# Performance work log

Hardware: AMD Instinct MI355X
Metric: run time of the kernel (lower is better)

Reference implementation:

```python
import jax, jax.numpy as jnp
import numpy as np

# Static pyramid config (must match setup_inputs' source_shape / level_start)
LEVEL_SHAPES = [(100, 100), (50, 50), (25, 25), (13, 13)]
DIM = 256
N_HEAD = 8
HEAD_DIM = DIM // N_HEAD
N_LEVEL = 4
N_POINT = 4
DIM_FF = 1024
B = 8
Q = 2048
LEN_IN = sum(h * w for h, w in LEVEL_SHAPES)


def layer_norm(x, g, b, eps=1e-5):
    m = jnp.mean(x, axis=-1, keepdims=True)
    v = jnp.mean(jnp.square(x - m), axis=-1, keepdims=True)
    return (x - m) * jax.lax.rsqrt(v + eps) * g + b


def bilinear_sample(v_flat, loc, H, W):
    # v_flat: (BH, H*W, hd); loc: (BH, Q, P, 2) normalized [0,1] as (x, y)
    # grid_sample align_corners=False with zero padding: pixel = loc*size - 0.5
    x = loc[..., 0] * W - 0.5
    y = loc[..., 1] * H - 0.5
    x0 = jnp.floor(x)
    y0 = jnp.floor(y)
    wx = (x - x0)[..., None]
    wy = (y - y0)[..., None]
    x0i = x0.astype(jnp.int32)
    y0i = y0.astype(jnp.int32)

    def gather(xi, yi):
        valid = ((xi >= 0) & (xi < W) & (yi >= 0) & (yi < H)).astype(v_flat.dtype)
        idx = jnp.clip(yi, 0, H - 1) * W + jnp.clip(xi, 0, W - 1)  # (BH,Q,P)
        BH, Qq, P = idx.shape
        f = jnp.take_along_axis(v_flat, idx.reshape(BH, Qq * P, 1), axis=1)
        return f.reshape(BH, Qq, P, -1) * valid[..., None]

    g00 = gather(x0i, y0i)
    g01 = gather(x0i + 1, y0i)
    g10 = gather(x0i, y0i + 1)
    g11 = gather(x0i + 1, y0i + 1)
    top = g00 * (1.0 - wx) + g01 * wx
    bot = g10 * (1.0 - wx) + g11 * wx
    return top * (1.0 - wy) + bot * wy


def ms_deform_attn_core(value, loc, attn):
    # value: (B, Lin, nh, hd); loc: (B, Q, nh, L, P, 2); attn: (B, Q, nh, L, P)
    Bv, Lin, nh, hd = value.shape
    Qq = loc.shape[1]
    out = jnp.zeros((Bv * nh, Qq, hd), value.dtype)
    start = 0
    for l, (H, W) in enumerate(LEVEL_SHAPES):
        v = value[:, start:start + H * W]                       # (B, HW, nh, hd)
        v = v.transpose(0, 2, 1, 3).reshape(Bv * nh, H * W, hd)
        ll = loc[:, :, :, l].transpose(0, 2, 1, 3, 4).reshape(Bv * nh, Qq, N_POINT, 2)
        aa = attn[:, :, :, l].transpose(0, 2, 1, 3).reshape(Bv * nh, Qq, N_POINT, 1)
        samp = bilinear_sample(v, ll, H, W)                     # (B*nh, Q, P, hd)
        out = out + jnp.sum(samp * aa, axis=2)
        start += H * W
    return out.reshape(Bv, nh, Qq, hd).transpose(0, 2, 1, 3).reshape(Bv, Qq, nh * hd)


def setup_inputs() -> dict:
    key = jax.random.key(0)
    ks = jax.random.split(key, 24)
    std = 0.02
    inp = {
        'input': jax.random.normal(ks[0], (B, Q, DIM), jnp.float32),
        'pos': jax.random.normal(ks[1], (B, Q, DIM), jnp.float32),
        'reference_point': jax.random.uniform(ks[2], (B, Q, N_LEVEL, 2), jnp.float32),
        'source': jax.random.normal(ks[3], (B, LEN_IN, DIM), jnp.float32),
        'source_shape': jnp.array(LEVEL_SHAPES, jnp.int64),
        'level_start': jnp.array(np.cumsum([0] + [h * w for h, w in LEVEL_SHAPES[:-1]]), jnp.int64),
        'source_mask': jnp.zeros((B, LEN_IN), jnp.bool_),
        # LayerNorms
        'ln1_g': jnp.ones((DIM,), jnp.float32), 'ln1_b': jnp.zeros((DIM,), jnp.float32),
        'ln2_g': jnp.ones((DIM,), jnp.float32), 'ln2_b': jnp.zeros((DIM,), jnp.float32),
        # MSDeformAttn projections
        'Wv': std * jax.random.normal(ks[4], (DIM, DIM), jnp.float32), 'bv': jnp.zeros((DIM,), jnp.float32),
        'Woff': std * jax.random.normal(ks[5], (DIM, N_HEAD * N_LEVEL * N_POINT * 2), jnp.float32),
        'boff': 0.5 * jax.random.normal(ks[6], (N_HEAD * N_LEVEL * N_POINT * 2,), jnp.float32),
        'Wattn': std * jax.random.normal(ks[7], (DIM, N_HEAD * N_LEVEL * N_POINT), jnp.float32),
        'battn': jnp.zeros((N_HEAD * N_LEVEL * N_POINT,), jnp.float32),
        'Wout': std * jax.random.normal(ks[8], (DIM, DIM), jnp.float32), 'bout': jnp.zeros((DIM,), jnp.float32),
        # FFN
        'W1': std * jax.random.normal(ks[9], (DIM, DIM_FF), jnp.float32), 'b1': jnp.zeros((DIM_FF,), jnp.float32),
        'W2': std * jax.random.normal(ks[10], (DIM_FF, DIM), jnp.float32), 'b2': jnp.zeros((DIM,), jnp.float32),
    }
    return inp


def reference(input, pos, reference_point, source, source_shape, level_start, source_mask,
              ln1_g, ln1_b, ln2_g, ln2_b, Wv, bv, Woff, boff, Wattn, battn, Wout, bout,
              W1, b1, W2, b2):
    # ---- cross norm + pos ----
    q = layer_norm(input, ln1_g, ln1_b)
    qp = q + pos
    # ---- MSDeformAttn ----
    value = source @ Wv + bv
    value = jnp.where(source_mask[..., None], 0.0, value)
    value = value.reshape(B, LEN_IN, N_HEAD, HEAD_DIM)
    offsets = (qp @ Woff + boff).reshape(B, Q, N_HEAD, N_LEVEL, N_POINT, 2)
    attn = (qp @ Wattn + battn).reshape(B, Q, N_HEAD, N_LEVEL * N_POINT)
    attn = jax.nn.softmax(attn, axis=-1).reshape(B, Q, N_HEAD, N_LEVEL, N_POINT)
    # offset normalizer is (W, H) per level
    normalizer = jnp.array([[w, h] for h, w in LEVEL_SHAPES], jnp.float32)
    loc = reference_point[:, :, None, :, None, :] + offsets / normalizer[None, None, None, :, None, :]
    out = ms_deform_attn_core(value, loc, attn)
    out = out @ Wout + bout
    x = input + out  # dropout is identity in eval
    # ---- FFN ----
    h = layer_norm(x, ln2_g, ln2_b)
    h = jax.nn.relu(h @ W1 + b1) @ W2 + b2
    x = x + h
    return (x, loc)
```

## Files before the change

kernel.cpp:

```cpp
#include <hip/hip_runtime.h>
#include <hip/hip_bf16.h>
#include <cstdint>
#include <cstddef>

#define B_    8
#define Q_    2048
#define DIM_  256
#define NH    8
#define HD    32
#define NL    4
#define NP    4
#define DFF   1024
#define LEN_IN_ 13294
#define MV    (B_*LEN_IN_)
#define MVPAD 106368
#define MQ    (B_*Q_)

typedef unsigned short u16;
typedef unsigned int   u32;
typedef __attribute__((ext_vector_type(8))) short short8;
typedef __attribute__((ext_vector_type(4))) float f32x4v;
typedef __attribute__((ext_vector_type(4))) unsigned short u16x4;

static __device__ __forceinline__ u16 f2bf(float f){
  union { float f; unsigned u; } x; x.f = f;
  unsigned r = x.u + 0x7fffu + ((x.u >> 16) & 1u);
  return (u16)(r >> 16);
}

#define GLDS(gp, lp) __builtin_amdgcn_global_load_lds( \
    (const __attribute__((address_space(1))) void*)(gp), \
    (__attribute__((address_space(3))) void*)(lp), 16, 0, 0)

template<int EPI, bool AF32>
__global__ __launch_bounds__(512, 4)
void gemm_k(const void* __restrict__ Ap, const u16* __restrict__ Bt,
            const float* __restrict__ bias, const float* __restrict__ res,
            void* __restrict__ outp, int N, int K, int Mstore)
{
  __shared__ u16 As[2][128*64];
  __shared__ u16 Bs[2][128*64];
  const int t = threadIdx.x;
  const int l = t & 63, wid = t >> 6;
  const int wm = wid >> 2, wn = wid & 3;
  const int m0 = blockIdx.x * 128, n0 = blockIdx.y * 128;

  f32x4v acc[4][2];
#pragma unroll
  for (int i = 0; i < 4; ++i)
#pragma unroll
    for (int j = 0; j < 2; ++j) acc[i][j] = 0.f;

  const int nkt = K >> 6;

  {
    float4 pa[4];
#pragma unroll
    for (int i = 0; i < 2; ++i) {
      const int chunk = i * 512 + t;
      const int row = chunk >> 3;
      const int sc = (chunk & 7) ^ (row & 7);
      if (AF32) {
        const int gr = m0 + row;
        float4 z = {0.f, 0.f, 0.f, 0.f};
        pa[2*i] = z; pa[2*i+1] = z;
        if (gr < Mstore) {
          const float* ga = (const float*)Ap + (size_t)gr * K + sc * 8;
          pa[2*i]   = *reinterpret_cast<const float4*>(ga);
          pa[2*i+1] = *reinterpret_cast<const float4*>(ga + 4);
        }
      } else {
        const u16* ga = (const u16*)Ap + (size_t)(m0 + row) * K + sc * 8;
        GLDS(ga, As[0] + chunk * 8);
      }
      const u16* gb = Bt + (size_t)(n0 + row) * K + sc * 8;
      GLDS(gb, Bs[0] + chunk * 8);
    }
    if (AF32) {
#pragma unroll
      for (int i = 0; i < 2; ++i) {
        const int chunk = i * 512 + t;
        short8 pk;
        pk[0]=(short)f2bf(pa[2*i].x);   pk[1]=(short)f2bf(pa[2*i].y);
        pk[2]=(short)f2bf(pa[2*i].z);   pk[3]=(short)f2bf(pa[2*i].w);
        pk[4]=(short)f2bf(pa[2*i+1].x); pk[5]=(short)f2bf(pa[2*i+1].y);
        pk[6]=(short)f2bf(pa[2*i+1].z); pk[7]=(short)f2bf(pa[2*i+1].w);
        *reinterpret_cast<short8*>(As[0] + chunk * 8) = pk;
      }
    }
    __syncthreads();
  }

  int cur = 0;
  for (int kt = 0; kt < nkt; ++kt) {
    const bool pf = (kt + 1 < nkt);
    float4 pa[4];
    if (pf) {
      const int kn = (kt + 1) * 64;
#pragma unroll
      for (int i = 0; i < 2; ++i) {
        const int chunk = i * 512 + t;
        const int row = chunk >> 3;
        const int sc = (chunk & 7) ^ (row & 7);
        if (AF32) {
          const int gr = m0 + row;
          float4 z = {0.f, 0.f, 0.f, 0.f};
          pa[2*i] = z; pa[2*i+1] = z;
          if (gr < Mstore) {
            const float* ga = (const float*)Ap + (size_t)gr * K + kn + sc * 8;
            pa[2*i]   = *reinterpret_cast<const float4*>(ga);
            pa[2*i+1] = *reinterpret_cast<const float4*>(ga + 4);
          }
        } else {
          const u16* ga = (const u16*)Ap + (size_t)(m0 + row) * K + kn + sc * 8;
          GLDS(ga, As[cur ^ 1] + chunk * 8);
        }
        const u16* gb = Bt + (size_t)(n0 + row) * K + kn + sc * 8;
        GLDS(gb, Bs[cur ^ 1] + chunk * 8);
      }
    }
#pragma unroll
    for (int kk = 0; kk < 2; ++kk) {
      short8 af[4], bfr[2];
      const int lr  = l & 15;
      const int c   = kk * 4 + (l >> 4);
      const int swz = c ^ (lr & 7);
#pragma unroll
      for (int mi = 0; mi < 4; ++mi) {
        int r = wm * 64 + mi * 16 + lr;
        af[mi] = *reinterpret_cast<const short8*>(As[cur] + (r * 8 + swz) * 8);
      }
#pragma unroll
      for (int ni = 0; ni < 2; ++ni) {
        int r = wn * 32 + ni * 16 + lr;
        bfr[ni] = *reinterpret_cast<const short8*>(Bs[cur] + (r * 8 + swz) * 8);
      }
#pragma unroll
      for (int mi = 0; mi < 4; ++mi)
#pragma unroll
        for (int ni = 0; ni < 2; ++ni)
          acc[mi][ni] = __builtin_amdgcn_mfma_f32_16x16x32_bf16(af[mi], bfr[ni], acc[mi][ni], 0, 0, 0);
    }
    if (pf && AF32) {
#pragma unroll
      for (int i = 0; i < 2; ++i) {
        const int chunk = i * 512 + t;
        short8 pk;
        pk[0]=(short)f2bf(pa[2*i].x);   pk[1]=(short)f2bf(pa[2*i].y);
        pk[2]=(short)f2bf(pa[2*i].z);   pk[3]=(short)f2bf(pa[2*i].w);
        pk[4]=(short)f2bf(pa[2*i+1].x); pk[5]=(short)f2bf(pa[2*i+1].y);
        pk[6]=(short)f2bf(pa[2*i+1].z); pk[7]=(short)f2bf(pa[2*i+1].w);
        *reinterpret_cast<short8*>(As[cur ^ 1] + chunk * 8) = pk;
      }
    }
    __syncthreads();
    cur ^= 1;
  }

  const int lr4 = l >> 4;
#pragma unroll
  for (int mi = 0; mi < 4; ++mi) {
    int rowb = m0 + wm * 64 + mi * 16 + lr4 * 4;
#pragma unroll
    for (int ni = 0; ni < 2; ++ni) {
      int col = n0 + wn * 32 + ni * 16 + (l & 15);
      float bb = bias[col];
#pragma unroll
      for (int v = 0; v < 4; ++v) {
        int r = rowb + v;
        if (r < Mstore) {
          float cv = acc[mi][ni][v] + bb;
          if (EPI == 2) cv += res[(size_t)r * N + col];
          if (EPI == 3) cv = fmaxf(cv, 0.f);
          if (EPI == 0 || EPI == 2) ((float*)outp)[(size_t)r * N + col] = cv;
          else                      ((u16*)outp)[(size_t)r * N + col] = f2bf(cv);
        }
      }
    }
  }
}

__global__ void prep_weights(const float* __restrict__ Wv,   const float* __restrict__ Woff,
                             const float* __restrict__ Wattn,const float* __restrict__ Wout,
                             const float* __restrict__ W1,   const float* __restrict__ W2,
                             const float* __restrict__ boff, const float* __restrict__ battn,
                             u16* __restrict__ WvT, u16* __restrict__ WcombT,
                             u16* __restrict__ WoutT, u16* __restrict__ W1T,
                             u16* __restrict__ W2T, float* __restrict__ bcomb)
{
  const int gid = blockIdx.x * 256 + threadIdx.x;
  const int R0 = 65536, R1 = R0 + 98304, R2 = R1 + 65536, R3 = R2 + 262144,
            R4 = R3 + 262144, R5 = R4 + 384;
  if (gid < R0) {
    int n = gid >> 8, k = gid & 255;
    WvT[gid] = f2bf(Wv[(size_t)k * 256 + n]);
  } else if (gid < R1) {
    int lo = gid - R0, n = lo >> 8, k = lo & 255;
    float s = (n < 256) ? Woff[(size_t)k * 256 + n] : Wattn[(size_t)k * 128 + (n - 256)];
    WcombT[lo] = f2bf(s);
  } else if (gid < R2) {
    int lo = gid - R1, n = lo >> 8, k = lo & 255;
    WoutT[lo] = f2bf(Wout[(size_t)k * 256 + n]);
  } else if (gid < R3) {
    int lo = gid - R2, n = lo >> 8, k = lo & 255;
    W1T[lo] = f2bf(W1[(size_t)k * 1024 + n]);
  } else if (gid < R4) {
    int lo = gid - R3, n = lo >> 10, k = lo & 1023;
    W2T[lo] = f2bf(W2[(size_t)k * 256 + n]);
  } else if (gid < R5) {
    int lo = gid - R4;
    bcomb[lo] = (lo < 256) ? boff[lo] : battn[lo - 256];
  }
}

template<bool ADDPOS>
__global__ __launch_bounds__(256)
void ln_k(const float* __restrict__ x, const float* __restrict__ pos,
          const float* __restrict__ g, const float* __restrict__ b, u16* __restrict__ out)
{
  const int warp = threadIdx.x >> 6, l = threadIdx.x & 63;
  const int row = blockIdx.x * 4 + warp;
  const float4 xv = reinterpret_cast<const float4*>(x + (size_t)row * 256)[l];
  float s = xv.x + xv.y + xv.z + xv.w;
#pragma unroll
  for (int o = 32; o; o >>= 1) s += __shfl_xor(s, o);
  const float mean = s * (1.f / 256.f);
  const float d0 = xv.x - mean, d1 = xv.y - mean, d2 = xv.z - mean, d3 = xv.w - mean;
  float vs = d0 * d0 + d1 * d1 + d2 * d2 + d3 * d3;
#pragma unroll
  for (int o = 32; o; o >>= 1) vs += __shfl_xor(vs, o);
  const float rs = rsqrtf(vs * (1.f / 256.f) + 1e-5f);
  const float4 gv = reinterpret_cast<const float4*>(g)[l];
  const float4 bv = reinterpret_cast<const float4*>(b)[l];
  float o0 = d0 * rs * gv.x + bv.x;
  float o1 = d1 * rs * gv.y + bv.y;
  float o2 = d2 * rs * gv.z + bv.z;
  float o3 = d3 * rs * gv.w + bv.w;
  if (ADDPOS) {
    const float4 pv = reinterpret_cast<const float4*>(pos + (size_t)row * 256)[l];
    o0 += pv.x; o1 += pv.y; o2 += pv.z; o3 += pv.w;
  }
  u16x4 ov; ov.x = f2bf(o0); ov.y = f2bf(o1); ov.z = f2bf(o2); ov.w = f2bf(o3);
  reinterpret_cast<u16x4*>(out + (size_t)row * 256)[l] = ov;
}

__global__ __launch_bounds__(256)
void msdeform_k(const u16* __restrict__ value, const float* __restrict__ oa,
                const float* __restrict__ refpt, float* __restrict__ locout,
                u16* __restrict__ outp)
{
  const int t = threadIdx.x;
  const int rloc = t >> 7;
  const int rem = t & 127;
  const int h = rem >> 4, p = rem & 15;
  const int row = blockIdx.x * 2 + rloc;
  const int b = row >> 11;
  const int lv = p >> 2;
  const float* orow = oa + (size_t)row * 384;

  const float araw = orow[256 + h * 16 + p];
  float mx = araw;
#pragma unroll
  for (int o = 1; o < 16; o <<= 1) mx = fmaxf(mx, __shfl_xor(mx, o, 16));
  const float e = __expf(araw - mx);
  float se = e;
#pragma unroll
  for (int o = 1; o < 16; o <<= 1) se += __shfl_xor(se, o, 16);
  const float aw = e / se;

  const float2 off = *reinterpret_cast<const float2*>(orow + h * 32 + p * 2);
  const float rn = (lv == 0) ? (1.f / 100.f) : (lv == 1) ? (1.f / 50.f)
                 : (lv == 2) ? (1.f / 25.f) : (1.f / 13.f);
  const float rx = refpt[(size_t)row * 8 + lv * 2 + 0];
  const float ry = refpt[(size_t)row * 8 + lv * 2 + 1];
  const float lx = rx + off.x * rn;
  const float ly = ry + off.y * rn;
  float2 lw; lw.x = lx; lw.y = ly;
  *reinterpret_cast<float2*>(locout + (((size_t)row * 8 + h) * 16 + p) * 2) = lw;

  const int Wl = (lv == 0) ? 100 : (lv == 1) ? 50 : (lv == 2) ? 25 : 13;
  const int st = (lv == 0) ? 0 : (lv == 1) ? 10000 : (lv == 2) ? 12500 : 13125;
  const float Wf = (float)Wl;
  const float xx = lx * Wf - 0.5f, yy = ly * Wf - 0.5f;
  const float xf = floorf(xx), yf = floorf(yy);
  const float wx = xx - xf, wy = yy - yf;
  const int x0 = (int)xf, y0 = (int)yf;
  const int xc0 = min(max(x0, 0), Wl - 1), xc1 = min(max(x0 + 1, 0), Wl - 1);
  const int yc0 = min(max(y0, 0), Wl - 1), yc1 = min(max(y0 + 1, 0), Wl - 1);
  const float vx0 = (x0 >= 0 && x0 < Wl) ? 1.f : 0.f;
  const float vx1 = (x0 + 1 >= 0 && x0 + 1 < Wl) ? 1.f : 0.f;
  const float vy0 = (y0 >= 0 && y0 < Wl) ? 1.f : 0.f;
  const float vy1 = (y0 + 1 >= 0 && y0 + 1 < Wl) ? 1.f : 0.f;
  const int o00 = st + yc0 * Wl + xc0, o01 = st + yc0 * Wl + xc1;
  const int o10 = st + yc1 * Wl + xc0, o11 = st + yc1 * Wl + xc1;
  const float w00 = aw * (1.f - wx) * (1.f - wy) * vx0 * vy0;
  const float w01 = aw * wx * (1.f - wy) * vx1 * vy0;
  const float w10 = aw * (1.f - wx) * wy * vx0 * vy1;
  const float w11 = aw * wx * wy * vx1 * vy1;

  const char* vbase = (const char*)value + (size_t)b * LEN_IN_ * 512 + (size_t)(h * 32 + p * 2) * 2;
  float a0 = 0.f, a1 = 0.f;
#pragma unroll
  for (int q = 0; q < 16; ++q) {
    const int   c00 = __shfl(o00, q, 16), c01 = __shfl(o01, q, 16);
    const int   c10 = __shfl(o10, q, 16), c11 = __shfl(o11, q, 16);
    const float u00 = __shfl(w00, q, 16), u01 = __shfl(w01, q, 16);
    const float u10 = __shfl(w10, q, 16), u11 = __shfl(w11, q, 16);
    const u32 g00 = *reinterpret_cast<const u32*>(vbase + (size_t)c00 * 512);
    const u32 g01 = *reinterpret_cast<const u32*>(vbase + (size_t)c01 * 512);
    const u32 g10 = *reinterpret_cast<const u32*>(vbase + (size_t)c10 * 512);
    const u32 g11 = *reinterpret_cast<const u32*>(vbase + (size_t)c11 * 512);
    union { u32 u; float f; } lo, hi;
    lo.u = g00 << 16; hi.u = g00 & 0xffff0000u; a0 += u00 * lo.f; a1 += u00 * hi.f;
    lo.u = g01 << 16; hi.u = g01 & 0xffff0000u; a0 += u01 * lo.f; a1 += u01 * hi.f;
    lo.u = g10 << 16; hi.u = g10 & 0xffff0000u; a0 += u10 * lo.f; a1 += u10 * hi.f;
    lo.u = g11 << 16; hi.u = g11 & 0xffff0000u; a0 += u11 * lo.f; a1 += u11 * hi.f;
  }
  const u32 res = ((u32)f2bf(a1) << 16) | (u32)f2bf(a0);
  reinterpret_cast<u32*>(outp)[(size_t)row * 128 + h * 16 + p] = res;
}

extern "C" void kernel_launch(void* const* d_in, const int* in_sizes, int n_in,
                              void* d_out, int out_size, void* d_ws, size_t ws_size,
                              hipStream_t stream)
{
  (void)in_sizes; (void)n_in; (void)out_size; (void)ws_size;
  const float* input  = (const float*)d_in[0];
  const float* pos    = (const float*)d_in[1];
  const float* refpt  = (const float*)d_in[2];
  const float* source = (const float*)d_in[3];
  const float* ln1_g  = (const float*)d_in[7];
  const float* ln1_b  = (const float*)d_in[8];
  const float* ln2_g  = (const float*)d_in[9];
  const float* ln2_b  = (const float*)d_in[10];
  const float* Wv     = (const float*)d_in[11];
  const float* bv     = (const float*)d_in[12];
  const float* Woff   = (const float*)d_in[13];
  const float* boff   = (const float*)d_in[14];
  const float* Wattn  = (const float*)d_in[15];
  const float* battn  = (const float*)d_in[16];
  const float* Wout   = (const float*)d_in[17];
  const float* bout   = (const float*)d_in[18];
  const float* W1     = (const float*)d_in[19];
  const float* b1     = (const float*)d_in[20];
  const float* W2     = (const float*)d_in[21];
  const float* b2     = (const float*)d_in[22];

  char* ws = (char*)d_ws;
  u16*   WvT    = (u16*)  (ws + 0);
  u16*   WcombT = (u16*)  (ws + 131072);
  u16*   WoutT  = (u16*)  (ws + 327680);
  u16*   W1T    = (u16*)  (ws + 458752);
  u16*   W2T    = (u16*)  (ws + 983040);
  float* bcomb  = (float*)(ws + 1507328);
  u16*   valueB = (u16*)  (ws + 1508864);
  u16*   hB     = (u16*)  (ws + 1508864);
  u16*   qpB    = (u16*)  (ws + 55969280);
  u16*   msout  = (u16*)  (ws + 55969280);
  float* oa     = (float*)(ws + 64357888);
  float* xbuf   = (float*)(ws + 89523712);
  u16*   xnB    = (u16*)  (ws + 106300928);

  float* out_x   = (float*)d_out;
  float* out_loc = (float*)d_out + (size_t)MQ * DIM_;

  hipLaunchKernelGGL(prep_weights, dim3(2946), dim3(256), 0, stream,
                     Wv, Woff, Wattn, Wout, W1, W2, boff, battn,
                     WvT, WcombT, WoutT, W1T, W2T, bcomb);

  hipLaunchKernelGGL((ln_k<true>), dim3(MQ / 4), dim3(256), 0, stream, input, pos, ln1_g, ln1_b, qpB);

  hipLaunchKernelGGL((gemm_k<1, true>), dim3(MVPAD / 128, 2), dim3(512), 0, stream,
                     (const void*)source, WvT, bv, (const float*)nullptr, (void*)valueB, 256, 256, MV);

  hipLaunchKernelGGL((gemm_k<0, false>), dim3(MQ / 128, 3), dim3(512), 0, stream,
                     (const void*)qpB, WcombT, bcomb, (const float*)nullptr, (void*)oa, 384, 256, MQ);

  hipLaunchKernelGGL(msdeform_k, dim3(MQ / 2), dim3(256), 0, stream,
                     valueB, oa, refpt, out_loc, msout);

  hipLaunchKernelGGL((gemm_k<2, false>), dim3(MQ / 128, 2), dim3(512), 0, stream,
                     (const void*)msout, WoutT, bout, input, (void*)xbuf, 256, 256, MQ);

  hipLaunchKernelGGL((ln_k<false>), dim3(MQ / 4), dim3(256), 0, stream, xbuf, (const float*)nullptr, ln2_g, ln2_b, xnB);

  hipLaunchKernelGGL((gemm_k<3, false>), dim3(MQ / 128, DFF / 128), dim3(512), 0, stream,
                     (const void*)xnB, W1T, b1, (const float*)nullptr, (void*)hB, DFF, 256, MQ);

  hipLaunchKernelGGL((gemm_k<2, false>), dim3(MQ / 128, 2), dim3(512), 0, stream,
                     (const void*)hB, W2T, b2, xbuf, (void*)out_x, 256, 1024, MQ);
}
```

Before: 413.7 us.

## Load A fragments directly to registers and stage B in large K chunks

The GEMM no longer stages A through LDS. Each lane loads its MFMA A fragment straight from global memory into registers and prefetches the next 32-wide K slice. B is staged into a single 128x256 LDS buffer per 256-wide K chunk, which cuts the number of barriers. This removes LDS traffic and sync for A, but the A global loads are now strided, B loads are no longer double-buffered, and the kernel waits on vmcnt(0) before each chunk.

```diff
diff --git a/kernel.cpp b/kernel.cpp
--- a/kernel.cpp
+++ b/kernel.cpp
@@ -38,11 +38,11 @@
             const float* __restrict__ bias, const float* __restrict__ res,
             void* __restrict__ outp, int N, int K, int Mstore)
 {
-  __shared__ u16 As[2][128*64];
-  __shared__ u16 Bs[2][128*64];
+  __shared__ u16 Bs[128 * 256];
   const int t = threadIdx.x;
   const int l = t & 63, wid = t >> 6;
   const int wm = wid >> 2, wn = wid & 3;
+  const int lr = l & 15, hi = l >> 4;
   const int m0 = blockIdx.x * 128, n0 = blockIdx.y * 128;
 
   f32x4v acc[4][2];
@@ -51,89 +51,85 @@
 #pragma unroll
     for (int j = 0; j < 2; ++j) acc[i][j] = 0.f;
 
-  const int nkt = K >> 6;
-
-  {
-    float4 pa[4];
-#pragma unroll
-    for (int i = 0; i < 2; ++i) {
+  const u16*   pA16[4];
+  const float* pA32[4];
+#pragma unroll
+  for (int mi = 0; mi < 4; ++mi) {
+    int r = m0 + wm * 64 + mi * 16 + lr;
+    r = (r < Mstore) ? r : (Mstore - 1);
+    if (AF32) pA32[mi] = (const float*)Ap + (size_t)r * K + hi * 8;
+    else      pA16[mi] = (const u16*)Ap + (size_t)r * K + hi * 8;
+  }
+
+  const int nchunk = K >> 8;
+  const int S = K >> 5;
+
+  short8 af[4];
+  short8 afn[4];
+  float4 pan[8];
+
+  if (AF32) {
+#pragma unroll
+    for (int mi = 0; mi < 4; ++mi) {
+      pan[2*mi]   = *reinterpret_cast<const float4*>(pA32[mi]);
+      pan[2*mi+1] = *reinterpret_cast<const float4*>(pA32[mi] + 4);
+    }
+  } else {
+#pragma unroll
+    for (int mi = 0; mi < 4; ++mi)
+      afn[mi] = *reinterpret_cast<const short8*>(pA16[mi]);
+  }
+
+  for (int ck = 0; ck < nchunk; ++ck) {
+    if (ck) __syncthreads();
+#pragma unroll
+    for (int i = 0; i < 8; ++i) {
       const int chunk = i * 512 + t;
-      const int row = chunk >> 3;
-      const int sc = (chunk & 7) ^ (row & 7);
+      const int row = chunk >> 5;
+      const int c16 = chunk & 31;
+      const int sc  = c16 ^ (row & 7);
+      GLDS(Bt + (size_t)(n0 + row) * K + ck * 256 + sc * 8, Bs + chunk * 8);
+    }
+    asm volatile("s_waitcnt vmcnt(0)" ::: "memory");
+    __syncthreads();
+
+#pragma unroll
+    for (int sl = 0; sl < 8; ++sl) {
+      const int s = ck * 8 + sl;
       if (AF32) {
-        const int gr = m0 + row;
-        float4 z = {0.f, 0.f, 0.f, 0.f};
-        pa[2*i] = z; pa[2*i+1] = z;
-        if (gr < Mstore) {
-          const float* ga = (const float*)Ap + (size_t)gr * K + sc * 8;
-          pa[2*i]   = *reinterpret_cast<const float4*>(ga);
-          pa[2*i+1] = *reinterpret_cast<const float4*>(ga + 4);
+#pragma unroll
+        for (int mi = 0; mi < 4; ++mi) {
+          short8 pk;
+          pk[0]=(short)f2bf(pan[2*mi].x);   pk[1]=(short)f2bf(pan[2*mi].y);
+          pk[2]=(short)f2bf(pan[2*mi].z);   pk[3]=(short)f2bf(pan[2*mi].w);
+          pk[4]=(short)f2bf(pan[2*mi+1].x); pk[5]=(short)f2bf(pan[2*mi+1].y);
+          pk[6]=(short)f2bf(pan[2*mi+1].z); pk[7]=(short)f2bf(pan[2*mi+1].w);
+          af[mi] = pk;
         }
       } else {
-        const u16* ga = (const u16*)Ap + (size_t)(m0 + row) * K + sc * 8;
-        GLDS(ga, As[0] + chunk * 8);
+#pragma unroll
+        for (int mi = 0; mi < 4; ++mi) af[mi] = afn[mi];
       }
-      const u16* gb = Bt + (size_t)(n0 + row) * K + sc * 8;
-      GLDS(gb, Bs[0] + chunk * 8);
-    }
-    if (AF32) {
-#pragma unroll
-      for (int i = 0; i < 2; ++i) {
-        const int chunk = i * 512 + t;
-        short8 pk;
-        pk[0]=(short)f2bf(pa[2*i].x);   pk[1]=(short)f2bf(pa[2*i].y);
-        pk[2]=(short)f2bf(pa[2*i].z);   pk[3]=(short)f2bf(pa[2*i].w);
-        pk[4]=(short)f2bf(pa[2*i+1].x); pk[5]=(short)f2bf(pa[2*i+1].y);
-        pk[6]=(short)f2bf(pa[2*i+1].z); pk[7]=(short)f2bf(pa[2*i+1].w);
-        *reinterpret_cast<short8*>(As[0] + chunk * 8) = pk;
-      }
-    }
-    __syncthreads();
-  }
-
-  int cur = 0;
-  for (int kt = 0; kt < nkt; ++kt) {
-    const bool pf = (kt + 1 < nkt);
-    float4 pa[4];
-    if (pf) {
-      const int kn = (kt + 1) * 64;
-#pragma unroll
-      for (int i = 0; i < 2; ++i) {
-        const int chunk = i * 512 + t;
-        const int row = chunk >> 3;
-        const int sc = (chunk & 7) ^ (row & 7);
+      if (s + 1 < S) {
+        const int ko = (s + 1) * 32;
         if (AF32) {
-          const int gr = m0 + row;
-          float4 z = {0.f, 0.f, 0.f, 0.f};
-          pa[2*i] = z; pa[2*i+1] = z;
-          if (gr < Mstore) {
-            const float* ga = (const float*)Ap + (size_t)gr * K + kn + sc * 8;
-            pa[2*i]   = *reinterpret_cast<const float4*>(ga);
-            pa[2*i+1] = *reinterpret_cast<const float4*>(ga + 4);
+#pragma unroll
+          for (int mi = 0; mi < 4; ++mi) {
+            pan[2*mi]   = *reinterpret_cast<const float4*>(pA32[mi] + ko);
+            pan[2*mi+1] = *reinterpret_cast<const float4*>(pA32[mi] + ko + 4);
           }
         } else {
-          const u16* ga = (const u16*)Ap + (size_t)(m0 + row) * K + kn + sc * 8;
-          GLDS(ga, As[cur ^ 1] + chunk * 8);
+#pragma unroll
+          for (int mi = 0; mi < 4; ++mi)
+            afn[mi] = *reinterpret_cast<const short8*>(pA16[mi] + ko);
         }
-        const u16* gb = Bt + (size_t)(n0 + row) * K + kn + sc * 8;
-        GLDS(gb, Bs[cur ^ 1] + chunk * 8);
       }
-    }
-#pragma unroll
-    for (int kk = 0; kk < 2; ++kk) {
-      short8 af[4], bfr[2];
-      const int lr  = l & 15;
-      const int c   = kk * 4 + (l >> 4);
-      const int swz = c ^ (lr & 7);
-#pragma unroll
-      for (int mi = 0; mi < 4; ++mi) {
-        int r = wm * 64 + mi * 16 + lr;
-        af[mi] = *reinterpret_cast<const short8*>(As[cur] + (r * 8 + swz) * 8);
-      }
+      short8 bfr[2];
 #pragma unroll
       for (int ni = 0; ni < 2; ++ni) {
-        int r = wn * 32 + ni * 16 + lr;
-        bfr[ni] = *reinterpret_cast<const short8*>(Bs[cur] + (r * 8 + swz) * 8);
+        const int r = wn * 32 + ni * 16 + lr;
+        const int c = (sl * 4 + hi) ^ (lr & 7);
+        bfr[ni] = *reinterpret_cast<const short8*>(Bs + (r * 32 + c) * 8);
       }
 #pragma unroll
       for (int mi = 0; mi < 4; ++mi)
@@ -141,29 +137,15 @@
         for (int ni = 0; ni < 2; ++ni)
           acc[mi][ni] = __builtin_amdgcn_mfma_f32_16x16x32_bf16(af[mi], bfr[ni], acc[mi][ni], 0, 0, 0);
     }
-    if (pf && AF32) {
-#pragma unroll
-      for (int i = 0; i < 2; ++i) {
-        const int chunk = i * 512 + t;
-        short8 pk;
-        pk[0]=(short)f2bf(pa[2*i].x);   pk[1]=(short)f2bf(pa[2*i].y);
-        pk[2]=(short)f2bf(pa[2*i].z);   pk[3]=(short)f2bf(pa[2*i].w);
-        pk[4]=(short)f2bf(pa[2*i+1].x); pk[5]=(short)f2bf(pa[2*i+1].y);
-        pk[6]=(short)f2bf(pa[2*i+1].z); pk[7]=(short)f2bf(pa[2*i+1].w);
-        *reinterpret_cast<short8*>(As[cur ^ 1] + chunk * 8) = pk;
-      }
-    }
-    __syncthreads();
-    cur ^= 1;
-  }
-
-  const int lr4 = l >> 4;
+  }
+
+  const int lr4 = hi;
 #pragma unroll
   for (int mi = 0; mi < 4; ++mi) {
     int rowb = m0 + wm * 64 + mi * 16 + lr4 * 4;
 #pragma unroll
     for (int ni = 0; ni < 2; ++ni) {
-      int col = n0 + wn * 32 + ni * 16 + (l & 15);
+      int col = n0 + wn * 32 + ni * 16 + lr;
       float bb = bias[col];
 #pragma unroll
       for (int v = 0; v < 4; ++v) {
```

Measured after the change: 599.0 us. +44.8%, slower.
